# Optimization experiments

Hardware: AMD Instinct MI355X
Metric: run time of the kernel (lower is better)

The kernel has to match this reference:

```python
import jax, jax.numpy as jnp
import numpy as np

E = 300   # embedding_dim
H = 300   # lstm hidden per direction
V = 200000
S = 128   # number of sentences
L = 128   # max sentence length
D = 2 * H # bilstm output dim == attention model_dim
NEG = -1e30


def setup_inputs() -> dict:
    key = jax.random.key(0)
    ks = jax.random.split(key, 12)
    sd = 0.05
    return {
        "tokens": jax.random.randint(ks[0], (S, L), 0, V, dtype=jnp.int32),
        "lengths": jax.random.randint(ks[1], (S,), 1, L + 1, dtype=jnp.int32),
        "table": jax.random.normal(ks[2], (V, E), jnp.float32) * sd,
        "Wih_f": jax.random.normal(ks[3], (4 * H, E), jnp.float32) * sd,
        "Whh_f": jax.random.normal(ks[4], (4 * H, H), jnp.float32) * sd,
        "bih_f": jax.random.normal(ks[5], (4 * H,), jnp.float32) * sd,
        "bhh_f": jax.random.normal(ks[6], (4 * H,), jnp.float32) * sd,
        "Wih_b": jax.random.normal(ks[7], (4 * H, E), jnp.float32) * sd,
        "Whh_b": jax.random.normal(ks[8], (4 * H, H), jnp.float32) * sd,
        "bih_b": jax.random.normal(ks[9], (4 * H,), jnp.float32) * sd,
        "bhh_b": jax.random.normal(ks[10], (4 * H,), jnp.float32) * sd,
    }


def _lstm_dir(x, Wih, Whh, bih, bhh, reverse):
    # x: [N, E] -> hs: [N, H]; PyTorch gate order (i, f, g, o)
    xw = x @ Wih.T + (bih + bhh)  # hoist input projection out of the scan

    def step(carry, xt):
        h, c = carry
        g = xt + h @ Whh.T
        i, f, gg, o = jnp.split(g, 4, axis=-1)
        c = jax.nn.sigmoid(f) * c + jax.nn.sigmoid(i) * jnp.tanh(gg)
        h = jax.nn.sigmoid(o) * jnp.tanh(c)
        return (h, c), h

    init = (jnp.zeros((H,), x.dtype), jnp.zeros((H,), x.dtype))
    _, hs = jax.lax.scan(step, init, xw, reverse=reverse)
    return hs


def reference(tokens, lengths, table, Wih_f, Whh_f, bih_f, bhh_f,
              Wih_b, Whh_b, bih_b, bhh_b):
    lens = np.asarray(lengths)                       # concrete lengths (static)
    rows = np.repeat(np.arange(S), lens)             # [N] sentence id per token
    cols = np.concatenate([np.arange(int(l)) for l in lens])  # [N] pos in sentence

    flat_ids = tokens[rows, cols]                    # ragged concat of all sentences, [N]
    embeds = table[flat_ids]                         # [N, E]

    # single BiLSTM pass over the whole concatenated token stream (batch=1)
    h_fwd = _lstm_dir(embeds, Wih_f, Whh_f, bih_f, bhh_f, reverse=False)
    h_bwd = _lstm_dir(embeds, Wih_b, Whh_b, bih_b, bhh_b, reverse=True)
    lstm_out = jnp.concatenate([h_fwd, h_bwd], axis=-1)  # [N, D]

    # scatter back to padded [S, L, D] so per-sentence attention is batched
    padded = jnp.zeros((S, L, D), lstm_out.dtype).at[rows, cols].set(lstm_out)
    mask = jnp.asarray(np.arange(L)[None, :] < lens[:, None])  # [S, L]

    # per-sentence scaled dot-product self-attention (Q=K=V=lstm_out slice)
    scores = jnp.einsum('sqd,skd->sqk', padded, padded) / jnp.sqrt(jnp.float32(D))
    scores = jnp.where(mask[:, None, :], scores, NEG)  # key padding mask
    attn = jax.nn.softmax(scores, axis=-1)
    ctx = jnp.einsum('sqk,skd->sqd', attn, padded)     # [S, L, D]

    # max-pool over valid positions of each sentence
    ctx = jnp.where(mask[:, :, None], ctx, NEG)
    return jnp.max(ctx, axis=1)                        # [S, D]
```

## Files before the change

### kernel.cpp

```cpp
#include <hip/hip_runtime.h>
#include <stdint.h>

#define S_ 128
#define L_ 128
#define E_ 300
#define H_ 300
#define NMAX (S_*L_)
#define R_ 1200
#define D_ 600
#define XW_STRIDE ((size_t)NMAX*R_)

__global__ void prep_kernel(const int* __restrict__ lengths, int* __restrict__ meta,
                            int* __restrict__ map, unsigned long long* __restrict__ hbuf) {
    __shared__ int offs[S_];
    int tid = threadIdx.x;
    if (tid == 0) {
        int acc = 0;
        for (int s = 0; s < S_; s++) { offs[s] = acc; acc += lengths[s]; }
        meta[0] = acc;
    }
    __syncthreads();
    for (int s = tid; s < S_; s += blockDim.x) {
        int o = offs[s], len = lengths[s];
        for (int l = 0; l < len; l++) map[o + l] = s * L_ + l;
    }
    for (int i = tid; i < 2*2*320; i += blockDim.x) hbuf[i] = 0ull;
}

__global__ __launch_bounds__(256, 1) void xw_kernel(
    const int* __restrict__ tokens, const float* __restrict__ table,
    const float* __restrict__ Wih_f, const float* __restrict__ bih_f, const float* __restrict__ bhh_f,
    const float* __restrict__ Wih_b, const float* __restrict__ bih_b, const float* __restrict__ bhh_b,
    const int* __restrict__ meta, const int* __restrict__ map, float* __restrict__ xw) {
    const int N = meta[0];
    const int n0 = blockIdx.x * 32;
    if (n0 >= N) return;
    const int r = blockIdx.y * 256 + threadIdx.x;
    const bool vr = (r < 2*R_);
    const int dir = (r >= R_) ? 1 : 0;
    const int rr = r - dir * R_;
    const float* W = dir ? Wih_b : Wih_f;
    float bias = 0.f;
    float4 w4[75];
    if (vr) {
        bias = dir ? (bih_b[rr] + bhh_b[rr]) : (bih_f[rr] + bhh_f[rr]);
        #pragma unroll
        for (int j = 0; j < 75; j++) w4[j] = *(const float4*)(W + (size_t)rr * E_ + 4*j);
    } else {
        #pragma unroll
        for (int j = 0; j < 75; j++) w4[j] = make_float4(0.f, 0.f, 0.f, 0.f);
    }
    float* xwd = xw + (size_t)dir * XW_STRIDE;
    const int iend = min(32, N - n0);
    for (int i = 0; i < iend; i++) {
        const int n = n0 + i;
        const int tok = tokens[map[n]];
        const float* arow = table + (size_t)tok * E_;
        float a0 = bias, a1 = 0.f, a2 = 0.f, a3 = 0.f;
        #pragma unroll
        for (int j = 0; j < 75; j++) {
            float4 a4 = *(const float4*)(arow + 4*j);
            a0 = fmaf(w4[j].x, a4.x, a0);
            a1 = fmaf(w4[j].y, a4.y, a1);
            a2 = fmaf(w4[j].z, a4.z, a2);
            a3 = fmaf(w4[j].w, a4.w, a3);
        }
        if (vr) xwd[(size_t)n * R_ + rr] = (a0 + a1) + (a2 + a3);
    }
}

__device__ __forceinline__ float sel4(int m, float a, float b, float c, float d) {
    float r = a;
    r = (m == 1) ? b : r;
    r = (m == 2) ? c : r;
    r = (m == 3) ? d : r;
    return r;
}
__device__ __forceinline__ float sigm(float x) {
    return __builtin_amdgcn_rcpf(1.f + __expf(-x));
}
__device__ __forceinline__ float tanh_fast(float x) {
    return 1.f - 2.f * __builtin_amdgcn_rcpf(1.f + __expf(2.f * x));
}

__global__ __launch_bounds__(256, 1) void scan_kernel(
    const float* __restrict__ Whh_f, const float* __restrict__ Whh_b,
    const int* __restrict__ meta, const int* __restrict__ map,
    unsigned long long* __restrict__ hbuf, const float* __restrict__ xw,
    float* __restrict__ padded) {
    const int N = meta[0];
    const int b = blockIdx.x;
    const int dir = b / 10;
    const int blk = b % 10;
    const int tid = threadIdx.x;
    const int wave = tid >> 6;
    const int lane = tid & 63;
    const int pair = tid >> 1;
    const int half = tid & 1;
    const int gate = pair & 3;
    const int d = 32 * blk + (pair >> 2);
    const bool vd = (d < H_);
    if (32 * blk + 8 * wave >= H_) return;

    const float* Whh = dir ? Whh_b : Whh_f;
    const int row = gate * H_ + (vd ? d : 0);
    const int cbase = half ? 148 : 0;
    float4 w4[38];
    if (vd) {
        const float* wr = Whh + (size_t)row * H_ + cbase;
        #pragma unroll
        for (int j = 0; j < 38; j++) w4[j] = *(const float4*)(wr + 4*j);
        if (half == 0) w4[37] = make_float4(0.f, 0.f, 0.f, 0.f);
    } else {
        #pragma unroll
        for (int j = 0; j < 38; j++) w4[j] = make_float4(0.f, 0.f, 0.f, 0.f);
    }
    const float* xwd = xw + (size_t)dir * XW_STRIDE;
    unsigned long long* hb = hbuf + dir * 2 * 320;

    __shared__ float hl[4][304];
    float* hw = hl[wave];

    float c = 0.f;
    int n0 = dir ? (N - 1) : 0;
    float xw_cur = vd ? xwd[(size_t)n0 * R_ + row] : 0.f;

    for (int t = 0; t < N; t++) {
        const int n = dir ? (N - 1 - t) : t;
        float xw_nxt = 0.f;
        if (vd && t + 1 < N) {
            const int nn = dir ? (N - 2 - t) : (t + 1);
            xw_nxt = xwd[(size_t)nn * R_ + row];
        }
        const int m = map[n];

        const unsigned long long* hp = hb + (size_t)(t & 1) * 320;
        const unsigned int want = (unsigned int)t;
        unsigned long long v0, v1, v2, v3, v4;
        for (;;) {
            v0 = __hip_atomic_load(hp + lane,        __ATOMIC_RELAXED, __HIP_MEMORY_SCOPE_AGENT);
            v1 = __hip_atomic_load(hp + 64  + lane,  __ATOMIC_RELAXED, __HIP_MEMORY_SCOPE_AGENT);
            v2 = __hip_atomic_load(hp + 128 + lane,  __ATOMIC_RELAXED, __HIP_MEMORY_SCOPE_AGENT);
            v3 = __hip_atomic_load(hp + 192 + lane,  __ATOMIC_RELAXED, __HIP_MEMORY_SCOPE_AGENT);
            v4 = (lane < 44) ? __hip_atomic_load(hp + 256 + lane, __ATOMIC_RELAXED, __HIP_MEMORY_SCOPE_AGENT)
                             : ((unsigned long long)want << 32);
            bool ok = ((unsigned int)(v0 >> 32) == want) &&
                      ((unsigned int)(v1 >> 32) == want) &&
                      ((unsigned int)(v2 >> 32) == want) &&
                      ((unsigned int)(v3 >> 32) == want) &&
                      ((unsigned int)(v4 >> 32) == want);
            if (ok) break;
        }
        hw[lane]        = __uint_as_float((unsigned int)v0);
        hw[64  + lane]  = __uint_as_float((unsigned int)v1);
        hw[128 + lane]  = __uint_as_float((unsigned int)v2);
        hw[192 + lane]  = __uint_as_float((unsigned int)v3);
        if (lane < 44) hw[256 + lane] = __uint_as_float((unsigned int)v4);

        const float* hbase = hw + cbase;
        float a0 = 0.f, a1 = 0.f, a2 = 0.f, a3 = 0.f;
        #pragma unroll
        for (int j = 0; j < 38; j++) {
            float4 h4 = *(const float4*)(hbase + 4*j);
            a0 = fmaf(w4[j].x, h4.x, a0);
            a1 = fmaf(w4[j].y, h4.y, a1);
            a2 = fmaf(w4[j].z, h4.z, a2);
            a3 = fmaf(w4[j].w, h4.w, a3);
        }
        float sum = (a0 + a1) + (a2 + a3);
        sum += __shfl_xor(sum, 1);
        const float acc = xw_cur + sum;

        const float aa = acc;
        const float bb = __shfl_xor(acc, 2);
        const float cc = __shfl_xor(acc, 4);
        const float dd = __shfl_xor(bb, 4);
        const float vi = sel4(gate,     aa, bb, cc, dd);
        const float vf = sel4(gate ^ 1, aa, bb, cc, dd);
        const float vg = sel4(gate ^ 2, aa, bb, cc, dd);
        const float vo = sel4(gate ^ 3, aa, bb, cc, dd);

        c = sigm(vf) * c + sigm(vi) * tanh_fast(vg);
        const float h = sigm(vo) * tanh_fast(c);

        if (vd && gate == 0 && half == 0) {
            padded[(size_t)m * D_ + dir * H_ + d] = h;
            const unsigned long long pv =
                ((unsigned long long)(unsigned int)(t + 1) << 32) |
                (unsigned long long)__float_as_uint(h);
            __hip_atomic_store(hb + (size_t)((t + 1) & 1) * 320 + d, pv,
                               __ATOMIC_RELAXED, __HIP_MEMORY_SCOPE_AGENT);
        }
        xw_cur = xw_nxt;
    }
}

__global__ __launch_bounds__(256) void attn_kernel(
    const int* __restrict__ lengths, const float* __restrict__ padded,
    float* __restrict__ out) {
    const int s = blockIdx.x;
    const int tid = threadIdx.x;
    const int Ls = lengths[s];
    const float* P = padded + (size_t)s * L_ * D_;
    __shared__ float sc[16][128];
    const float scale = 0.040824829046386304f;
    float vmax0 = -1e30f, vmax1 = -1e30f, vmax2 = -1e30f;

    const int nqt = (Ls + 15) / 16;
    for (int qt = 0; qt < nqt; qt++) {
        const int q0 = qt * 16;
        if (tid < 128) {
            float acc[16];
            #pragma unroll
            for (int i = 0; i < 16; i++) acc[i] = -1e30f;
            if (tid < Ls) {
                #pragma unroll
                for (int i = 0; i < 16; i++) acc[i] = 0.f;
                const float* pk = P + (size_t)tid * D_;
                for (int e4 = 0; e4 < 150; e4++) {
                    const float4 k4 = *(const float4*)(pk + 4*e4);
                    #pragma unroll
                    for (int i = 0; i < 16; i++) {
                        const float4 q4 = *(const float4*)(P + (size_t)(q0 + i) * D_ + 4*e4);
                        acc[i] = fmaf(k4.x, q4.x, acc[i]);
                        acc[i] = fmaf(k4.y, q4.y, acc[i]);
                        acc[i] = fmaf(k4.z, q4.z, acc[i]);
                        acc[i] = fmaf(k4.w, q4.w, acc[i]);
                    }
                }
                #pragma unroll
                for (int i = 0; i < 16; i++) acc[i] *= scale;
            }
            #pragma unroll
            for (int i = 0; i < 16; i++) sc[i][tid] = acc[i];
        }
        __syncthreads();

        {
            const int w = tid >> 6, l = tid & 63;
            #pragma unroll
            for (int ii = 0; ii < 4; ii++) {
                const int i = w * 4 + ii;
                float x0 = sc[i][l], x1 = sc[i][64 + l];
                float mx = fmaxf(x0, x1);
                #pragma unroll
                for (int off = 32; off; off >>= 1) mx = fmaxf(mx, __shfl_xor(mx, off));
                float e0 = expf(x0 - mx), e1 = expf(x1 - mx);
                float sm = e0 + e1;
                #pragma unroll
                for (int off = 32; off; off >>= 1) sm += __shfl_xor(sm, off);
                const float inv = 1.f / sm;
                sc[i][l] = e0 * inv;
                sc[i][64 + l] = e1 * inv;
            }
        }
        __syncthreads();

        #pragma unroll
        for (int j = 0; j < 3; j++) {
            const int dd = j * 256 + tid;
            if (dd < D_) {
                float ca[16];
                #pragma unroll
                for (int i = 0; i < 16; i++) ca[i] = 0.f;
                for (int k4 = 0; k4 < 32; k4++) {
                    const float p0 = P[(size_t)(4*k4 + 0) * D_ + dd];
                    const float p1 = P[(size_t)(4*k4 + 1) * D_ + dd];
                    const float p2 = P[(size_t)(4*k4 + 2) * D_ + dd];
                    const float p3 = P[(size_t)(4*k4 + 3) * D_ + dd];
                    #pragma unroll
                    for (int i = 0; i < 16; i++) {
                        const float4 pr = *(const float4*)(&sc[i][4*k4]);
                        ca[i] = fmaf(pr.x, p0, ca[i]);
                        ca[i] = fmaf(pr.y, p1, ca[i]);
                        ca[i] = fmaf(pr.z, p2, ca[i]);
                        ca[i] = fmaf(pr.w, p3, ca[i]);
                    }
                }
                float vm = (j == 0) ? vmax0 : (j == 1) ? vmax1 : vmax2;
                #pragma unroll
                for (int i = 0; i < 16; i++)
                    if (q0 + i < Ls) vm = fmaxf(vm, ca[i]);
                if (j == 0) vmax0 = vm; else if (j == 1) vmax1 = vm; else vmax2 = vm;
            }
        }
        __syncthreads();
    }
    if (tid < D_)        out[(size_t)s * D_ + tid] = vmax0;
    if (256 + tid < D_)  out[(size_t)s * D_ + 256 + tid] = vmax1;
    if (512 + tid < D_)  out[(size_t)s * D_ + 512 + tid] = vmax2;
}

extern "C" void kernel_launch(void* const* d_in, const int* in_sizes, int n_in,
                              void* d_out, int out_size, void* d_ws, size_t ws_size,
                              hipStream_t stream) {
    const int*   tokens  = (const int*)d_in[0];
    const int*   lengths = (const int*)d_in[1];
    const float* table   = (const float*)d_in[2];
    const float* Wih_f   = (const float*)d_in[3];
    const float* Whh_f   = (const float*)d_in[4];
    const float* bih_f   = (const float*)d_in[5];
    const float* bhh_f   = (const float*)d_in[6];
    const float* Wih_b   = (const float*)d_in[7];
    const float* Whh_b   = (const float*)d_in[8];
    const float* bih_b   = (const float*)d_in[9];
    const float* bhh_b   = (const float*)d_in[10];
    float* out = (float*)d_out;

    char* ws = (char*)d_ws;
    int* meta                 = (int*)(ws + 0);
    int* map                  = (int*)(ws + 256);
    unsigned long long* hbuf  = (unsigned long long*)(ws + 256 + 65536);
    float* xw                 = (float*)(ws + 256 + 65536 + 10240);
    float* padded             = (float*)(ws + 256 + 65536 + 10240 + (size_t)2*NMAX*R_*4);

    prep_kernel<<<1, 256, 0, stream>>>(lengths, meta, map, hbuf);
    xw_kernel<<<dim3(NMAX/32, 10), 256, 0, stream>>>(tokens, table,
        Wih_f, bih_f, bhh_f, Wih_b, bih_b, bhh_b, meta, map, xw);
    scan_kernel<<<20, 256, 0, stream>>>(Whh_f, Whh_b, meta, map, hbuf, xw, padded);
    attn_kernel<<<S_, 256, 0, stream>>>(lengths, padded, out);
}
```

Before: 19.73 ms.

## Split LSTM scan dot products four ways across lanes and batch xw/padded I/O

Redistributes the recurrent scan over 38 blocks instead of 20, with each gate row's 300-length dot product split across four lanes (19 float4 registers each) rather than two. This halves the per-step serial FMA chain and per-thread register footprint. It also prefetches eight timesteps of xw and map values at once and defers the padded stores until after each 8-step group, taking global memory traffic off the critical recurrence path. The cost is more blocks polling the shared h buffer each step, which may add contention on the cross-block handshake.

After: 23.61 ms. +19.6%, slower.

```diff
diff --git a/kernel.cpp b/kernel.cpp
--- a/kernel.cpp
+++ b/kernel.cpp
@@ -90,108 +90,122 @@
     float* __restrict__ padded) {
     const int N = meta[0];
     const int b = blockIdx.x;
-    const int dir = b / 10;
-    const int blk = b % 10;
+    const int dir = b / 19;
+    const int blk = b % 19;
     const int tid = threadIdx.x;
     const int wave = tid >> 6;
     const int lane = tid & 63;
-    const int pair = tid >> 1;
-    const int half = tid & 1;
-    const int gate = pair & 3;
-    const int d = 32 * blk + (pair >> 2);
-    const bool vd = (d < H_);
-    if (32 * blk + 8 * wave >= H_) return;
+    const int q    = lane & 3;
+    const int gate = (lane >> 2) & 3;
+    const int dloc = lane >> 4;
+    const int d = blk * 16 + wave * 4 + dloc;
+    if (blk * 16 + wave * 4 >= H_) return;
 
     const float* Whh = dir ? Whh_b : Whh_f;
-    const int row = gate * H_ + (vd ? d : 0);
-    const int cbase = half ? 148 : 0;
-    float4 w4[38];
-    if (vd) {
+    const int row = gate * H_ + d;
+    const int cbase = q * 76;
+    float4 w4[19];
+    {
         const float* wr = Whh + (size_t)row * H_ + cbase;
         #pragma unroll
-        for (int j = 0; j < 38; j++) w4[j] = *(const float4*)(wr + 4*j);
-        if (half == 0) w4[37] = make_float4(0.f, 0.f, 0.f, 0.f);
-    } else {
-        #pragma unroll
-        for (int j = 0; j < 38; j++) w4[j] = make_float4(0.f, 0.f, 0.f, 0.f);
+        for (int j = 0; j < 18; j++) w4[j] = *(const float4*)(wr + 4*j);
+        w4[18] = (q == 3) ? make_float4(0.f, 0.f, 0.f, 0.f)
+                          : *(const float4*)(wr + 72);
     }
     const float* xwd = xw + (size_t)dir * XW_STRIDE;
     unsigned long long* hb = hbuf + dir * 2 * 320;
 
     __shared__ float hl[4][304];
     float* hw = hl[wave];
+    if (lane < 4) hw[300 + lane] = 0.f;
 
     float c = 0.f;
-    int n0 = dir ? (N - 1) : 0;
-    float xw_cur = vd ? xwd[(size_t)n0 * R_ + row] : 0.f;
-
-    for (int t = 0; t < N; t++) {
-        const int n = dir ? (N - 1 - t) : t;
-        float xw_nxt = 0.f;
-        if (vd && t + 1 < N) {
-            const int nn = dir ? (N - 2 - t) : (t + 1);
-            xw_nxt = xwd[(size_t)nn * R_ + row];
-        }
-        const int m = map[n];
-
-        const unsigned long long* hp = hb + (size_t)(t & 1) * 320;
-        const unsigned int want = (unsigned int)t;
-        unsigned long long v0, v1, v2, v3, v4;
-        for (;;) {
-            v0 = __hip_atomic_load(hp + lane,        __ATOMIC_RELAXED, __HIP_MEMORY_SCOPE_AGENT);
-            v1 = __hip_atomic_load(hp + 64  + lane,  __ATOMIC_RELAXED, __HIP_MEMORY_SCOPE_AGENT);
-            v2 = __hip_atomic_load(hp + 128 + lane,  __ATOMIC_RELAXED, __HIP_MEMORY_SCOPE_AGENT);
-            v3 = __hip_atomic_load(hp + 192 + lane,  __ATOMIC_RELAXED, __HIP_MEMORY_SCOPE_AGENT);
-            v4 = (lane < 44) ? __hip_atomic_load(hp + 256 + lane, __ATOMIC_RELAXED, __HIP_MEMORY_SCOPE_AGENT)
-                             : ((unsigned long long)want << 32);
-            bool ok = ((unsigned int)(v0 >> 32) == want) &&
-                      ((unsigned int)(v1 >> 32) == want) &&
-                      ((unsigned int)(v2 >> 32) == want) &&
-                      ((unsigned int)(v3 >> 32) == want) &&
-                      ((unsigned int)(v4 >> 32) == want);
-            if (ok) break;
-        }
-        hw[lane]        = __uint_as_float((unsigned int)v0);
-        hw[64  + lane]  = __uint_as_float((unsigned int)v1);
-        hw[128 + lane]  = __uint_as_float((unsigned int)v2);
-        hw[192 + lane]  = __uint_as_float((unsigned int)v3);
-        if (lane < 44) hw[256 + lane] = __uint_as_float((unsigned int)v4);
-
-        const float* hbase = hw + cbase;
-        float a0 = 0.f, a1 = 0.f, a2 = 0.f, a3 = 0.f;
-        #pragma unroll
-        for (int j = 0; j < 38; j++) {
-            float4 h4 = *(const float4*)(hbase + 4*j);
-            a0 = fmaf(w4[j].x, h4.x, a0);
-            a1 = fmaf(w4[j].y, h4.y, a1);
-            a2 = fmaf(w4[j].z, h4.z, a2);
-            a3 = fmaf(w4[j].w, h4.w, a3);
-        }
-        float sum = (a0 + a1) + (a2 + a3);
-        sum += __shfl_xor(sum, 1);
-        const float acc = xw_cur + sum;
-
-        const float aa = acc;
-        const float bb = __shfl_xor(acc, 2);
-        const float cc = __shfl_xor(acc, 4);
-        const float dd = __shfl_xor(bb, 4);
-        const float vi = sel4(gate,     aa, bb, cc, dd);
-        const float vf = sel4(gate ^ 1, aa, bb, cc, dd);
-        const float vg = sel4(gate ^ 2, aa, bb, cc, dd);
-        const float vo = sel4(gate ^ 3, aa, bb, cc, dd);
-
-        c = sigm(vf) * c + sigm(vi) * tanh_fast(vg);
-        const float h = sigm(vo) * tanh_fast(c);
-
-        if (vd && gate == 0 && half == 0) {
-            padded[(size_t)m * D_ + dir * H_ + d] = h;
-            const unsigned long long pv =
-                ((unsigned long long)(unsigned int)(t + 1) << 32) |
-                (unsigned long long)__float_as_uint(h);
-            __hip_atomic_store(hb + (size_t)((t + 1) & 1) * 320 + d, pv,
-                               __ATOMIC_RELAXED, __HIP_MEMORY_SCOPE_AGENT);
-        }
-        xw_cur = xw_nxt;
+    const bool storer = (gate == 0 && q == 0);
+
+    for (int t8 = 0; t8 < N; t8 += 8) {
+        float xq[8];
+        int   mq[8];
+        #pragma unroll
+        for (int k = 0; k < 8; k++) {
+            const int t = t8 + k;
+            const int n = dir ? (N - 1 - t) : t;
+            xq[k] = (t < N) ? xwd[(size_t)n * R_ + row] : 0.f;
+            mq[k] = (t < N) ? map[n] : 0;
+        }
+        float xh[8];
+
+        #pragma unroll
+        for (int k = 0; k < 8; k++) {
+            const int t = t8 + k;
+            if (t < N) {
+                const unsigned long long* hp = hb + (size_t)(t & 1) * 320;
+                const unsigned int want = (unsigned int)t;
+                unsigned long long v0, v1, v2, v3, v4;
+                for (;;) {
+                    v0 = __hip_atomic_load(hp + lane,        __ATOMIC_RELAXED, __HIP_MEMORY_SCOPE_AGENT);
+                    v1 = __hip_atomic_load(hp + 64  + lane,  __ATOMIC_RELAXED, __HIP_MEMORY_SCOPE_AGENT);
+                    v2 = __hip_atomic_load(hp + 128 + lane,  __ATOMIC_RELAXED, __HIP_MEMORY_SCOPE_AGENT);
+                    v3 = __hip_atomic_load(hp + 192 + lane,  __ATOMIC_RELAXED, __HIP_MEMORY_SCOPE_AGENT);
+                    v4 = (lane < 44) ? __hip_atomic_load(hp + 256 + lane, __ATOMIC_RELAXED, __HIP_MEMORY_SCOPE_AGENT)
+                                     : ((unsigned long long)want << 32);
+                    bool ok = ((unsigned int)(v0 >> 32) == want) &&
+                              ((unsigned int)(v1 >> 32) == want) &&
+                              ((unsigned int)(v2 >> 32) == want) &&
+                              ((unsigned int)(v3 >> 32) == want) &&
+                              ((unsigned int)(v4 >> 32) == want);
+                    if (ok) break;
+                }
+                hw[lane]        = __uint_as_float((unsigned int)v0);
+                hw[64  + lane]  = __uint_as_float((unsigned int)v1);
+                hw[128 + lane]  = __uint_as_float((unsigned int)v2);
+                hw[192 + lane]  = __uint_as_float((unsigned int)v3);
+                if (lane < 44) hw[256 + lane] = __uint_as_float((unsigned int)v4);
+
+                const float* hbase = hw + cbase;
+                float a0 = 0.f, a1 = 0.f, a2 = 0.f, a3 = 0.f;
+                #pragma unroll
+                for (int j = 0; j < 19; j++) {
+                    float4 h4 = *(const float4*)(hbase + 4*j);
+                    a0 = fmaf(w4[j].x, h4.x, a0);
+                    a1 = fmaf(w4[j].y, h4.y, a1);
+                    a2 = fmaf(w4[j].z, h4.z, a2);
+                    a3 = fmaf(w4[j].w, h4.w, a3);
+                }
+                float sum = (a0 + a1) + (a2 + a3);
+                sum += __shfl_xor(sum, 1);
+                sum += __shfl_xor(sum, 2);
+                const float acc = xq[k] + sum;
+
+                const float aa = acc;
+                const float bb = __shfl_xor(acc, 4);
+                const float cc = __shfl_xor(acc, 8);
+                const float dd = __shfl_xor(bb, 8);
+                const float vi = sel4(gate,     aa, bb, cc, dd);
+                const float vf = sel4(gate ^ 1, aa, bb, cc, dd);
+                const float vg = sel4(gate ^ 2, aa, bb, cc, dd);
+                const float vo = sel4(gate ^ 3, aa, bb, cc, dd);
+
+                c = sigm(vf) * c + sigm(vi) * tanh_fast(vg);
+                const float h = sigm(vo) * tanh_fast(c);
+                xh[k] = h;
+
+                if (storer) {
+                    const unsigned long long pv =
+                        ((unsigned long long)(unsigned int)(t + 1) << 32) |
+                        (unsigned long long)__float_as_uint(h);
+                    __hip_atomic_store(hb + (size_t)((t + 1) & 1) * 320 + d, pv,
+                                       __ATOMIC_RELAXED, __HIP_MEMORY_SCOPE_AGENT);
+                }
+            }
+        }
+
+        if (storer) {
+            #pragma unroll
+            for (int k = 0; k < 8; k++) {
+                if (t8 + k < N)
+                    padded[(size_t)mq[k] * D_ + dir * H_ + d] = xh[k];
+            }
+        }
     }
 }
 
@@ -317,6 +331,6 @@
     prep_kernel<<<1, 256, 0, stream>>>(lengths, meta, map, hbuf);
     xw_kernel<<<dim3(NMAX/32, 10), 256, 0, stream>>>(tokens, table,
         Wih_f, bih_f, bhh_f, Wih_b, bih_b, bhh_b, meta, map, xw);
-    scan_kernel<<<20, 256, 0, stream>>>(Whh_f, Whh_b, meta, map, hbuf, xw, padded);
+    scan_kernel<<<38, 256, 0, stream>>>(Whh_f, Whh_b, meta, map, hbuf, xw, padded);
     attn_kernel<<<S_, 256, 0, stream>>>(lengths, padded, out);
 }
```

## Unroll LSTM scan by four with batched xw prefetch and deferred output stores

Applied to the files above, without the earlier changes.

The recurrent scan loop now processes four timesteps per iteration. It prefetches the four input-projection values and map entries up front, and defers the padded-output stores until after the block of steps, so global memory traffic leaves the serial handshake path. Weights are now loaded as 152 scalar registers through volatile loads instead of float4, and launch bounds are expressed via amdgpu attributes. The change risks more register pressure and spills, and slower scalar volatile loads at weight setup.

Result: slower. 22.60 ms (+14.5%).

```diff
diff --git a/kernel.cpp b/kernel.cpp
--- a/kernel.cpp
+++ b/kernel.cpp
@@ -83,8 +83,9 @@
     return 1.f - 2.f * __builtin_amdgcn_rcpf(1.f + __expf(2.f * x));
 }
 
-__global__ __launch_bounds__(256, 1) void scan_kernel(
-    const float* __restrict__ Whh_f, const float* __restrict__ Whh_b,
+__global__ __attribute__((amdgpu_flat_work_group_size(256, 256), amdgpu_waves_per_eu(1, 1)))
+void scan_kernel(
+    const float* Whh_f, const float* Whh_b,
     const int* __restrict__ meta, const int* __restrict__ map,
     unsigned long long* __restrict__ hbuf, const float* __restrict__ xw,
     float* __restrict__ padded) {
@@ -105,93 +106,112 @@
     const float* Whh = dir ? Whh_b : Whh_f;
     const int row = gate * H_ + (vd ? d : 0);
     const int cbase = half ? 148 : 0;
-    float4 w4[38];
-    if (vd) {
-        const float* wr = Whh + (size_t)row * H_ + cbase;
-        #pragma unroll
-        for (int j = 0; j < 38; j++) w4[j] = *(const float4*)(wr + 4*j);
-        if (half == 0) w4[37] = make_float4(0.f, 0.f, 0.f, 0.f);
-    } else {
-        #pragma unroll
-        for (int j = 0; j < 38; j++) w4[j] = make_float4(0.f, 0.f, 0.f, 0.f);
-    }
+    const int wcnt  = half ? 152 : 148;
+
+    float w[152];
+    {
+        const volatile float* wr = Whh + (size_t)row * H_ + cbase;
+        #pragma unroll
+        for (int j = 0; j < 152; j++) w[j] = (j < wcnt) ? wr[j] : 0.f;
+        if (!vd) {
+            #pragma unroll
+            for (int j = 0; j < 152; j++) w[j] = 0.f;
+        }
+    }
+
     const float* xwd = xw + (size_t)dir * XW_STRIDE;
     unsigned long long* hb = hbuf + dir * 2 * 320;
 
     __shared__ float hl[4][304];
     float* hw = hl[wave];
+    if (lane < 4) hw[300 + lane] = 0.f;
 
     float c = 0.f;
-    int n0 = dir ? (N - 1) : 0;
-    float xw_cur = vd ? xwd[(size_t)n0 * R_ + row] : 0.f;
-
-    for (int t = 0; t < N; t++) {
-        const int n = dir ? (N - 1 - t) : t;
-        float xw_nxt = 0.f;
-        if (vd && t + 1 < N) {
-            const int nn = dir ? (N - 2 - t) : (t + 1);
-            xw_nxt = xwd[(size_t)nn * R_ + row];
-        }
-        const int m = map[n];
-
-        const unsigned long long* hp = hb + (size_t)(t & 1) * 320;
-        const unsigned int want = (unsigned int)t;
-        unsigned long long v0, v1, v2, v3, v4;
-        for (;;) {
-            v0 = __hip_atomic_load(hp + lane,        __ATOMIC_RELAXED, __HIP_MEMORY_SCOPE_AGENT);
-            v1 = __hip_atomic_load(hp + 64  + lane,  __ATOMIC_RELAXED, __HIP_MEMORY_SCOPE_AGENT);
-            v2 = __hip_atomic_load(hp + 128 + lane,  __ATOMIC_RELAXED, __HIP_MEMORY_SCOPE_AGENT);
-            v3 = __hip_atomic_load(hp + 192 + lane,  __ATOMIC_RELAXED, __HIP_MEMORY_SCOPE_AGENT);
-            v4 = (lane < 44) ? __hip_atomic_load(hp + 256 + lane, __ATOMIC_RELAXED, __HIP_MEMORY_SCOPE_AGENT)
-                             : ((unsigned long long)want << 32);
-            bool ok = ((unsigned int)(v0 >> 32) == want) &&
-                      ((unsigned int)(v1 >> 32) == want) &&
-                      ((unsigned int)(v2 >> 32) == want) &&
-                      ((unsigned int)(v3 >> 32) == want) &&
-                      ((unsigned int)(v4 >> 32) == want);
-            if (ok) break;
-        }
-        hw[lane]        = __uint_as_float((unsigned int)v0);
-        hw[64  + lane]  = __uint_as_float((unsigned int)v1);
-        hw[128 + lane]  = __uint_as_float((unsigned int)v2);
-        hw[192 + lane]  = __uint_as_float((unsigned int)v3);
-        if (lane < 44) hw[256 + lane] = __uint_as_float((unsigned int)v4);
-
-        const float* hbase = hw + cbase;
-        float a0 = 0.f, a1 = 0.f, a2 = 0.f, a3 = 0.f;
-        #pragma unroll
-        for (int j = 0; j < 38; j++) {
-            float4 h4 = *(const float4*)(hbase + 4*j);
-            a0 = fmaf(w4[j].x, h4.x, a0);
-            a1 = fmaf(w4[j].y, h4.y, a1);
-            a2 = fmaf(w4[j].z, h4.z, a2);
-            a3 = fmaf(w4[j].w, h4.w, a3);
-        }
-        float sum = (a0 + a1) + (a2 + a3);
-        sum += __shfl_xor(sum, 1);
-        const float acc = xw_cur + sum;
-
-        const float aa = acc;
-        const float bb = __shfl_xor(acc, 2);
-        const float cc = __shfl_xor(acc, 4);
-        const float dd = __shfl_xor(bb, 4);
-        const float vi = sel4(gate,     aa, bb, cc, dd);
-        const float vf = sel4(gate ^ 1, aa, bb, cc, dd);
-        const float vg = sel4(gate ^ 2, aa, bb, cc, dd);
-        const float vo = sel4(gate ^ 3, aa, bb, cc, dd);
-
-        c = sigm(vf) * c + sigm(vi) * tanh_fast(vg);
-        const float h = sigm(vo) * tanh_fast(c);
-
-        if (vd && gate == 0 && half == 0) {
-            padded[(size_t)m * D_ + dir * H_ + d] = h;
-            const unsigned long long pv =
-                ((unsigned long long)(unsigned int)(t + 1) << 32) |
-                (unsigned long long)__float_as_uint(h);
-            __hip_atomic_store(hb + (size_t)((t + 1) & 1) * 320 + d, pv,
-                               __ATOMIC_RELAXED, __HIP_MEMORY_SCOPE_AGENT);
-        }
-        xw_cur = xw_nxt;
+    const bool storer = (gate == 0 && half == 0);
+
+    for (int t4 = 0; t4 < N; t4 += 4) {
+        float xq[4];
+        int   mq[4];
+        #pragma unroll
+        for (int k = 0; k < 4; k++) {
+            const int tc = min(t4 + k, N - 1);
+            const int n = dir ? (N - 1 - tc) : tc;
+            xq[k] = xwd[(size_t)n * R_ + row];
+            mq[k] = map[n];
+        }
+        float xh[4];
+
+        #pragma unroll
+        for (int k = 0; k < 4; k++) {
+            const int t = t4 + k;
+            if (t < N) {
+                const unsigned long long* hp = hb + (size_t)(t & 1) * 320;
+                const unsigned int want = (unsigned int)t;
+                unsigned long long v0, v1, v2, v3, v4;
+                for (;;) {
+                    v0 = __hip_atomic_load(hp + lane,        __ATOMIC_RELAXED, __HIP_MEMORY_SCOPE_AGENT);
+                    v1 = __hip_atomic_load(hp + 64  + lane,  __ATOMIC_RELAXED, __HIP_MEMORY_SCOPE_AGENT);
+                    v2 = __hip_atomic_load(hp + 128 + lane,  __ATOMIC_RELAXED, __HIP_MEMORY_SCOPE_AGENT);
+                    v3 = __hip_atomic_load(hp + 192 + lane,  __ATOMIC_RELAXED, __HIP_MEMORY_SCOPE_AGENT);
+                    v4 = (lane < 44) ? __hip_atomic_load(hp + 256 + lane, __ATOMIC_RELAXED, __HIP_MEMORY_SCOPE_AGENT)
+                                     : ((unsigned long long)want << 32);
+                    bool ok = ((unsigned int)(v0 >> 32) == want) &&
+                              ((unsigned int)(v1 >> 32) == want) &&
+                              ((unsigned int)(v2 >> 32) == want) &&
+                              ((unsigned int)(v3 >> 32) == want) &&
+                              ((unsigned int)(v4 >> 32) == want);
+                    if (ok) break;
+                }
+                hw[lane]        = __uint_as_float((unsigned int)v0);
+                hw[64  + lane]  = __uint_as_float((unsigned int)v1);
+                hw[128 + lane]  = __uint_as_float((unsigned int)v2);
+                hw[192 + lane]  = __uint_as_float((unsigned int)v3);
+                if (lane < 44) hw[256 + lane] = __uint_as_float((unsigned int)v4);
+
+                const float* hbase = hw + cbase;
+                float a0 = 0.f, a1 = 0.f, a2 = 0.f, a3 = 0.f;
+                #pragma unroll
+                for (int j = 0; j < 38; j++) {
+                    float4 h4 = *(const float4*)(hbase + 4*j);
+                    a0 = fmaf(w[4*j + 0], h4.x, a0);
+                    a1 = fmaf(w[4*j + 1], h4.y, a1);
+                    a2 = fmaf(w[4*j + 2], h4.z, a2);
+                    a3 = fmaf(w[4*j + 3], h4.w, a3);
+                }
+                float sum = (a0 + a1) + (a2 + a3);
+                sum += __shfl_xor(sum, 1);
+                const float acc = xq[k] + sum;
+
+                const float aa = acc;
+                const float bb = __shfl_xor(acc, 2);
+                const float cc = __shfl_xor(acc, 4);
+                const float dd = __shfl_xor(bb, 4);
+                const float vi = sel4(gate,     aa, bb, cc, dd);
+                const float vf = sel4(gate ^ 1, aa, bb, cc, dd);
+                const float vg = sel4(gate ^ 2, aa, bb, cc, dd);
+                const float vo = sel4(gate ^ 3, aa, bb, cc, dd);
+
+                c = sigm(vf) * c + sigm(vi) * tanh_fast(vg);
+                const float h = sigm(vo) * tanh_fast(c);
+                xh[k] = h;
+
+                if (vd && storer) {
+                    const unsigned long long pv =
+                        ((unsigned long long)(unsigned int)(t + 1) << 32) |
+                        (unsigned long long)__float_as_uint(h);
+                    __hip_atomic_store(hb + (size_t)((t + 1) & 1) * 320 + d, pv,
+                                       __ATOMIC_RELAXED, __HIP_MEMORY_SCOPE_AGENT);
+                }
+            }
+        }
+
+        if (vd && storer) {
+            #pragma unroll
+            for (int k = 0; k < 4; k++) {
+                if (t4 + k < N)
+                    padded[(size_t)mq[k] * D_ + dir * H_ + d] = xh[k];
+            }
+        }
     }
 }
 
```
